# Optimization experiments

Hardware: AMD Instinct MI355X
Metric: run time of the kernel (lower is better)

Reference implementation:

```python
import jax, jax.numpy as jnp
import numpy as np

# dims per module source / chosen globals
B, LB = 4, 28            # new frames, buffered frames; M = B+LB = L = 32
DK, DV = 256, 32         # Dk=256 hardcoded; Dv = 4*len_of_lookup+4 with len_of_lookup=7
HS, WS = 64, 64          # H//8, W//8 with H=W=512
LMAX = 32                # memory cap L
TRAIN_SZ = 1000          # log base train_sz
ALPHA = 0.5              # blend coefficient (original inits 0, which zeroes the branch)
# log(L*h*w + h*w, train_sz) / sqrt(Dk)
SCALE = float(np.log(LMAX * HS * WS + HS * WS) / np.log(TRAIN_SZ) / np.sqrt(DK))


def _xavier(key, fan_in, fan_out):
    lim = np.sqrt(6.0 / (fan_in + fan_out))
    return jax.random.uniform(key, (fan_in, fan_out), jnp.float32, -lim, lim)


def setup_inputs() -> dict:
    key = jax.random.key(0)
    ks = jax.random.split(key, 7)
    return {
        "fc": jax.random.normal(ks[0], (B, DK, HS, WS), jnp.float32),
        "fm": jax.random.normal(ks[1], (B, DV, HS, WS), jnp.float32),
        "key_buffer": jax.random.normal(ks[2], (LB, DK, HS, WS), jnp.float32),
        "value_buffer": jax.random.normal(ks[3], (LB, DV, HS, WS), jnp.float32),
        "Q": _xavier(ks[4], DK, DK),
        "K": _xavier(ks[5], DK, DK),
        "V": _xavier(ks[6], DV, DV),
    }


def reference(fc, fm, key_buffer, value_buffer, Q, K, V):
    # matmul = einsum('ijkl,jm->imkl'): per-pixel channel mixing
    q = jnp.einsum('bdhw,de->behw', fc, Q)                      # [B,Dk,h,w]
    k = jnp.concatenate([jnp.einsum('bdhw,de->behw', fc, K), key_buffer], axis=0)    # [M,Dk,h,w]
    v = jnp.concatenate([jnp.einsum('bdhw,de->behw', fm, V), value_buffer], axis=0)  # [M,Dv,h,w]
    # current_batch (=1) < L, so no slicing of k/v on this step
    scores = SCALE * jnp.einsum('bdhw,mdhw->bmhw', q, k)        # [B,M,h,w]
    attn = jax.nn.softmax(scores, axis=-1)                      # NOTE: softmax over width axis, as in source (dim=-1)
    ctx = jnp.einsum('bmhw,mdhw->bdhw', attn, v)                # [B,Dv,h,w]
    return fm + ALPHA * ctx
```

## Files before the change

### kernel.cpp

```cpp
#include <hip/hip_runtime.h>
#include <hip/hip_bf16.h>
#include <cmath>

#define NB 4
#define NM 32
#define DKc 256
#define DVc 32
#define NP 4096

using bf16x8 = __attribute__((ext_vector_type(8))) short;
using f32x4  = __attribute__((ext_vector_type(4))) float;
using f32x2  = __attribute__((ext_vector_type(2))) float;

__device__ __forceinline__ unsigned short f2bf(float f) {
    union { float f; unsigned u; } x; x.f = f;
    unsigned r = 0x7FFFu + ((x.u >> 16) & 1u);
    return (unsigned short)((x.u + r) >> 16);
}

__global__ __launch_bounds__(256) void k_prep(
    const float* __restrict__ fc, unsigned short* __restrict__ fcT,
    const float* __restrict__ Q, unsigned short* __restrict__ WTq,
    const float* __restrict__ K, unsigned short* __restrict__ WTk,
    const float* __restrict__ fm, const float* __restrict__ V, float* __restrict__ vproj) {
    int x = blockIdx.x;
    int t = threadIdx.x;
    if (x < 1056) {
        __shared__ float tile[64][65];
        const float* s; unsigned short* d; int R, C, r0, c0;
        if (x < 1024) {
            int bb = x >> 8, rest = x & 255;
            R = 256; C = 4096;
            r0 = (rest >> 6) * 64; c0 = (rest & 63) * 64;
            s = fc + (long)bb * 256 * 4096; d = fcT + (long)bb * 256 * 4096;
        } else {
            int i = x - 1024;
            int mat = i >> 4, idx = i & 15;
            R = 256; C = 256;
            r0 = (idx >> 2) * 64; c0 = (idx & 3) * 64;
            s = mat ? K : Q; d = mat ? WTk : WTq;
        }
        #pragma unroll
        for (int j = 0; j < 16; ++j) {
            int i = t + 256 * j;
            int r = i >> 6, c = i & 63;
            tile[r][c] = s[(long)(r0 + r) * C + c0 + c];
        }
        __syncthreads();
        #pragma unroll
        for (int j = 0; j < 8; ++j) {
            int i = t + 256 * j;
            int row = i >> 5;
            int pr = i & 31;
            float f0 = tile[2 * pr][row];
            float f1 = tile[2 * pr + 1][row];
            unsigned pack = (unsigned)f2bf(f0) | ((unsigned)f2bf(f1) << 16);
            reinterpret_cast<unsigned*>(d)[(((long)(c0 + row) * R + r0) >> 1) + pr] = pack;
        }
    } else {
        __shared__ float Vl[32][32];
        __shared__ float fml[32][256];
        int i = x - 1056;
        int b = i >> 4, p0 = (i & 15) * 256;
        #pragma unroll
        for (int j = 0; j < 4; ++j) { int ii = t + 256 * j; Vl[ii >> 5][ii & 31] = V[ii]; }
        for (int j = 0; j < 32; ++j) {
            int ii = t + 256 * j;
            int dd = ii >> 8, c = ii & 255;
            fml[dd][c] = fm[((long)b * DVc + dd) * NP + p0 + c];
        }
        __syncthreads();
        float acc[32];
        #pragma unroll
        for (int e = 0; e < 32; ++e) acc[e] = 0.f;
        for (int dd = 0; dd < 32; ++dd) {
            float fv = fml[dd][t];
            #pragma unroll
            for (int e = 0; e < 32; ++e) acc[e] += fv * Vl[dd][e];
        }
        #pragma unroll
        for (int e = 0; e < 32; ++e) vproj[((long)b * DVc + e) * NP + p0 + t] = acc[e];
    }
}

__global__ __launch_bounds__(256) void k_proj(
    const unsigned short* __restrict__ WTq, const unsigned short* __restrict__ WTk,
    const unsigned short* __restrict__ fcT,
    float* __restrict__ qproj, float* __restrict__ kproj) {
    int t = threadIdx.x;
    int wave = t >> 6, lane = t & 63;
    int y = blockIdx.y;
    int b = y & 3, mat = y >> 2;
    int p0 = blockIdx.x * 64;
    int ln = lane & 15, quad = lane >> 4;
    const unsigned short* WT = mat ? WTk : WTq;
    float* dst = mat ? kproj : qproj;
    int e0w = wave * 64;
    const unsigned short* bbase = fcT + ((long)b * NP + p0 + ln) * DKc + quad * 8;
    f32x4 acc[4][4] = {};
    for (int kk = 0; kk < DKc; kk += 32) {
        bf16x8 a[4], bb[4];
        #pragma unroll
        for (int i = 0; i < 4; ++i)
            a[i] = *reinterpret_cast<const bf16x8*>(WT + (long)(e0w + i * 16 + ln) * DKc + quad * 8 + kk);
        #pragma unroll
        for (int j = 0; j < 4; ++j)
            bb[j] = *reinterpret_cast<const bf16x8*>(bbase + (long)j * 16 * DKc + kk);
        #pragma unroll
        for (int i = 0; i < 4; ++i)
            #pragma unroll
            for (int j = 0; j < 4; ++j)
                acc[i][j] = __builtin_amdgcn_mfma_f32_16x16x32_bf16(a[i], bb[j], acc[i][j], 0, 0, 0);
    }
    #pragma unroll
    for (int i = 0; i < 4; ++i)
        #pragma unroll
        for (int j = 0; j < 4; ++j)
            #pragma unroll
            for (int r = 0; r < 4; ++r) {
                int e = e0w + i * 16 + quad * 4 + r, p = p0 + j * 16 + ln;
                dst[((long)b * DKc + e) * NP + p] = acc[i][j][r];
            }
}

__global__ __launch_bounds__(256, 2) void k_scores(
    const float* __restrict__ qproj, const float* __restrict__ kproj,
    const float* __restrict__ kbuf, float* __restrict__ partial) {
    int t = threadIdx.x;
    int wseg = blockIdx.x, ec = blockIdx.y, mq = blockIdx.z;
    int w0 = wseg * 512 + t * 2;
    int e0 = ec * 32;
    const float* kp[4];
    #pragma unroll
    for (int mi = 0; mi < 4; ++mi) {
        int m = mq * 4 + mi;
        kp[mi] = (m < 4 ? kproj + (long)m * DKc * NP : kbuf + (long)(m - 4) * DKc * NP)
                 + (long)e0 * NP + w0;
    }
    const float* qp[4];
    #pragma unroll
    for (int b = 0; b < 4; ++b)
        qp[b] = qproj + ((long)b * DKc + e0) * NP + w0;

    f32x2 acc[4][4];
    #pragma unroll
    for (int b = 0; b < 4; ++b)
        #pragma unroll
        for (int mi = 0; mi < 4; ++mi) acc[b][mi] = (f32x2){0.f, 0.f};

    for (int e4 = 0; e4 < 32; e4 += 4) {
        f32x2 qv[4][4], kv[4][4];
        #pragma unroll
        for (int u = 0; u < 4; ++u) {
            long off = (long)(e4 + u) * NP;
            #pragma unroll
            for (int b = 0; b < 4; ++b)
                qv[u][b] = *reinterpret_cast<const f32x2*>(qp[b] + off);
            #pragma unroll
            for (int mi = 0; mi < 4; ++mi)
                kv[u][mi] = *reinterpret_cast<const f32x2*>(kp[mi] + off);
        }
        #pragma unroll
        for (int u = 0; u < 4; ++u)
            #pragma unroll
            for (int b = 0; b < 4; ++b)
                #pragma unroll
                for (int mi = 0; mi < 4; ++mi)
                    acc[b][mi] += qv[u][b] * kv[u][mi];
    }
    #pragma unroll
    for (int b = 0; b < 4; ++b)
        #pragma unroll
        for (int mi = 0; mi < 4; ++mi) {
            float* pp = partial + (((long)b * 8 + ec) * NM + mq * 4 + mi) * NP + w0;
            *reinterpret_cast<f32x2*>(pp) = acc[b][mi];
        }
}

__global__ __launch_bounds__(512) void k_out(
    const float* __restrict__ partial, const float* __restrict__ vproj,
    const float* __restrict__ vbuf, const float* __restrict__ fm,
    float* __restrict__ out, float scale) {
    __shared__ float sc[32][68];
    int t = threadIdx.x;
    int b = blockIdx.x >> 6, hrow = blockIdx.x & 63;
    int p0h = hrow * 64;
    int wave = t >> 6, lane = t & 63;
    {
        int w = t & 63, mg = t >> 6;
        float s[4] = {0.f, 0.f, 0.f, 0.f};
        #pragma unroll
        for (int c = 0; c < 8; ++c) {
            const float* pp = partial + (((long)b * 8 + c) * NM + mg * 4) * NP + p0h + w;
            #pragma unroll
            for (int mi = 0; mi < 4; ++mi) s[mi] += pp[(long)mi * NP];
        }
        #pragma unroll
        for (int mi = 0; mi < 4; ++mi) sc[mg * 4 + mi][w] = s[mi] * scale;
    }
    __syncthreads();
    #pragma unroll
    for (int r = 0; r < 4; ++r) {
        int m = wave * 4 + r;
        float x = sc[m][lane];
        float mx = x;
        #pragma unroll
        for (int d = 1; d < 64; d <<= 1) mx = fmaxf(mx, __shfl_xor(mx, d));
        float e = __expf(x - mx);
        float sum = e;
        #pragma unroll
        for (int d = 1; d < 64; d <<= 1) sum += __shfl_xor(sum, d);
        sc[m][lane] = e / sum;
    }
    __syncthreads();
    {
        int dg = t >> 6, w = t & 63;
        float c4[4] = {0.f, 0.f, 0.f, 0.f};
        #pragma unroll
        for (int m = 0; m < NM; ++m) {
            float a = sc[m][w];
            const float* vp = (m < 4 ? vproj + (long)m * DVc * NP : vbuf + (long)(m - 4) * DVc * NP)
                              + (long)(dg * 4) * NP + p0h + w;
            #pragma unroll
            for (int i = 0; i < 4; ++i) c4[i] += a * vp[(long)i * NP];
        }
        #pragma unroll
        for (int i = 0; i < 4; ++i) {
            long gi = ((long)b * DVc + dg * 4 + i) * NP + p0h + w;
            out[gi] = fm[gi] + 0.5f * c4[i];
        }
    }
}

extern "C" void kernel_launch(void* const* d_in, const int* in_sizes, int n_in,
                              void* d_out, int out_size, void* d_ws, size_t ws_size,
                              hipStream_t stream) {
    const float* fc = (const float*)d_in[0];
    const float* fm = (const float*)d_in[1];
    const float* kb = (const float*)d_in[2];
    const float* vb = (const float*)d_in[3];
    const float* Q  = (const float*)d_in[4];
    const float* K  = (const float*)d_in[5];
    const float* V  = (const float*)d_in[6];
    float* out = (float*)d_out;
    char* ws = (char*)d_ws;
    float*          qproj = (float*)(ws);
    float*          kproj = (float*)(ws + 16777216);
    float*          vproj = (float*)(ws + 33554432);
    unsigned short* fcT   = (unsigned short*)(ws + 35651584);
    unsigned short* WTq   = (unsigned short*)(ws + 44040192);
    unsigned short* WTk   = (unsigned short*)(ws + 44171264);
    float*          partial = (float*)(ws + 35651584);
    float scale = (float)(log(135168.0) / log(1000.0) / 16.0);

    hipLaunchKernelGGL(k_prep, dim3(1120), dim3(256), 0, stream,
                       fc, fcT, Q, WTq, K, WTk, fm, V, vproj);
    hipLaunchKernelGGL(k_proj, dim3(64, 8), dim3(256), 0, stream,
                       WTq, WTk, fcT, qproj, kproj);
    hipLaunchKernelGGL(k_scores, dim3(8, 8, 8), dim3(256), 0, stream,
                       qproj, kproj, kb, partial);
    hipLaunchKernelGGL(k_out, dim3(256), dim3(512), 0, stream,
                       partial, vproj, vb, fm, out, scale);
}
```

Measured before the change: 244.5 us.

## Fuse score computation, softmax and value aggregation into a single kernel

Replaces the separate scores kernel, which wrote split-K partial sums to workspace, and the output kernel with one fused kernel. Each 1024-thread block handles one (batch, row) pair. It stages that row's query projection in shared memory and computes the full 256-deep dot products against all 32 memory keys, two keys per wave. It then applies the width softmax and aggregates values. This removes the partial-score round trip through global memory and one launch. The cost is that the key tensors are re-read once per batch index rather than shared across batches, and the grid is only 256 large blocks.

```diff
diff --git a/kernel.cpp b/kernel.cpp
--- a/kernel.cpp
+++ b/kernel.cpp
@@ -123,111 +123,89 @@
             }
 }
 
-__global__ __launch_bounds__(256, 2) void k_scores(
+__global__ __launch_bounds__(1024) void k_fused(
     const float* __restrict__ qproj, const float* __restrict__ kproj,
-    const float* __restrict__ kbuf, float* __restrict__ partial) {
-    int t = threadIdx.x;
-    int wseg = blockIdx.x, ec = blockIdx.y, mq = blockIdx.z;
-    int w0 = wseg * 512 + t * 2;
-    int e0 = ec * 32;
-    const float* kp[4];
-    #pragma unroll
-    for (int mi = 0; mi < 4; ++mi) {
-        int m = mq * 4 + mi;
-        kp[mi] = (m < 4 ? kproj + (long)m * DKc * NP : kbuf + (long)(m - 4) * DKc * NP)
-                 + (long)e0 * NP + w0;
-    }
-    const float* qp[4];
-    #pragma unroll
-    for (int b = 0; b < 4; ++b)
-        qp[b] = qproj + ((long)b * DKc + e0) * NP + w0;
-
-    f32x2 acc[4][4];
-    #pragma unroll
-    for (int b = 0; b < 4; ++b)
-        #pragma unroll
-        for (int mi = 0; mi < 4; ++mi) acc[b][mi] = (f32x2){0.f, 0.f};
-
-    for (int e4 = 0; e4 < 32; e4 += 4) {
-        f32x2 qv[4][4], kv[4][4];
-        #pragma unroll
-        for (int u = 0; u < 4; ++u) {
-            long off = (long)(e4 + u) * NP;
-            #pragma unroll
-            for (int b = 0; b < 4; ++b)
-                qv[u][b] = *reinterpret_cast<const f32x2*>(qp[b] + off);
-            #pragma unroll
-            for (int mi = 0; mi < 4; ++mi)
-                kv[u][mi] = *reinterpret_cast<const f32x2*>(kp[mi] + off);
-        }
-        #pragma unroll
-        for (int u = 0; u < 4; ++u)
-            #pragma unroll
-            for (int b = 0; b < 4; ++b)
-                #pragma unroll
-                for (int mi = 0; mi < 4; ++mi)
-                    acc[b][mi] += qv[u][b] * kv[u][mi];
-    }
-    #pragma unroll
-    for (int b = 0; b < 4; ++b)
-        #pragma unroll
-        for (int mi = 0; mi < 4; ++mi) {
-            float* pp = partial + (((long)b * 8 + ec) * NM + mq * 4 + mi) * NP + w0;
-            *reinterpret_cast<f32x2*>(pp) = acc[b][mi];
-        }
-}
-
-__global__ __launch_bounds__(512) void k_out(
-    const float* __restrict__ partial, const float* __restrict__ vproj,
+    const float* __restrict__ kbuf, const float* __restrict__ vproj,
     const float* __restrict__ vbuf, const float* __restrict__ fm,
     float* __restrict__ out, float scale) {
-    __shared__ float sc[32][68];
+    __shared__ float smem[256 * 64];
     int t = threadIdx.x;
     int b = blockIdx.x >> 6, hrow = blockIdx.x & 63;
-    int p0h = hrow * 64;
+    int p0 = hrow * 64;
     int wave = t >> 6, lane = t & 63;
+
     {
-        int w = t & 63, mg = t >> 6;
-        float s[4] = {0.f, 0.f, 0.f, 0.f};
-        #pragma unroll
-        for (int c = 0; c < 8; ++c) {
-            const float* pp = partial + (((long)b * 8 + c) * NM + mg * 4) * NP + p0h + w;
-            #pragma unroll
-            for (int mi = 0; mi < 4; ++mi) s[mi] += pp[(long)mi * NP];
-        }
-        #pragma unroll
-        for (int mi = 0; mi < 4; ++mi) sc[mg * 4 + mi][w] = s[mi] * scale;
+        const float* qbase = qproj + (long)b * DKc * NP + p0;
+        #pragma unroll
+        for (int j = 0; j < 16; ++j) {
+            int i = t + 1024 * j;
+            int e = i >> 6, w = i & 63;
+            smem[e * 64 + w] = qbase[(long)e * NP + w];
+        }
+    }
+    __syncthreads();
+
+    float attnw[2];
+    {
+        const float* kp[2];
+        #pragma unroll
+        for (int mi = 0; mi < 2; ++mi) {
+            int m = wave * 2 + mi;
+            kp[mi] = (m < 4 ? kproj + (long)m * DKc * NP : kbuf + (long)(m - 4) * DKc * NP)
+                     + p0 + lane;
+        }
+        float s[2] = {0.f, 0.f};
+        for (int e8 = 0; e8 < 256; e8 += 8) {
+            float qv[8], kv[8][2];
+            #pragma unroll
+            for (int u = 0; u < 8; ++u) qv[u] = smem[(e8 + u) * 64 + lane];
+            #pragma unroll
+            for (int u = 0; u < 8; ++u)
+                #pragma unroll
+                for (int mi = 0; mi < 2; ++mi)
+                    kv[u][mi] = kp[mi][(long)u * NP];
+            #pragma unroll
+            for (int u = 0; u < 8; ++u)
+                #pragma unroll
+                for (int mi = 0; mi < 2; ++mi)
+                    s[mi] += qv[u] * kv[u][mi];
+            #pragma unroll
+            for (int mi = 0; mi < 2; ++mi) kp[mi] += 8 * NP;
+        }
+        #pragma unroll
+        for (int mi = 0; mi < 2; ++mi) {
+            float x = s[mi] * scale;
+            float mx = x;
+            #pragma unroll
+            for (int d = 1; d < 64; d <<= 1) mx = fmaxf(mx, __shfl_xor(mx, d));
+            float ev = __expf(x - mx);
+            float sum = ev;
+            #pragma unroll
+            for (int d = 1; d < 64; d <<= 1) sum += __shfl_xor(sum, d);
+            attnw[mi] = ev / sum;
+        }
     }
     __syncthreads();
     #pragma unroll
-    for (int r = 0; r < 4; ++r) {
-        int m = wave * 4 + r;
-        float x = sc[m][lane];
-        float mx = x;
-        #pragma unroll
-        for (int d = 1; d < 64; d <<= 1) mx = fmaxf(mx, __shfl_xor(mx, d));
-        float e = __expf(x - mx);
-        float sum = e;
-        #pragma unroll
-        for (int d = 1; d < 64; d <<= 1) sum += __shfl_xor(sum, d);
-        sc[m][lane] = e / sum;
-    }
+    for (int mi = 0; mi < 2; ++mi)
+        smem[(wave * 2 + mi) * 68 + lane] = attnw[mi];
     __syncthreads();
+
     {
         int dg = t >> 6, w = t & 63;
-        float c4[4] = {0.f, 0.f, 0.f, 0.f};
+        float c2[2] = {0.f, 0.f};
         #pragma unroll
         for (int m = 0; m < NM; ++m) {
-            float a = sc[m][w];
+            float a = smem[m * 68 + w];
             const float* vp = (m < 4 ? vproj + (long)m * DVc * NP : vbuf + (long)(m - 4) * DVc * NP)
-                              + (long)(dg * 4) * NP + p0h + w;
-            #pragma unroll
-            for (int i = 0; i < 4; ++i) c4[i] += a * vp[(long)i * NP];
-        }
-        #pragma unroll
-        for (int i = 0; i < 4; ++i) {
-            long gi = ((long)b * DVc + dg * 4 + i) * NP + p0h + w;
-            out[gi] = fm[gi] + 0.5f * c4[i];
+                              + (long)(dg * 2) * NP + p0 + w;
+            #pragma unroll
+            for (int i = 0; i < 2; ++i) c2[i] += a * vp[(long)i * NP];
+        }
+        #pragma unroll
+        for (int i = 0; i < 2; ++i) {
+            long gi = ((long)b * DVc + dg * 2 + i) * NP + p0 + w;
+            out[gi] = fm[gi] + 0.5f * c2[i];
         }
     }
 }
@@ -250,15 +228,12 @@
     unsigned short* fcT   = (unsigned short*)(ws + 35651584);
     unsigned short* WTq   = (unsigned short*)(ws + 44040192);
     unsigned short* WTk   = (unsigned short*)(ws + 44171264);
-    float*          partial = (float*)(ws + 35651584);
     float scale = (float)(log(135168.0) / log(1000.0) / 16.0);
 
     hipLaunchKernelGGL(k_prep, dim3(1120), dim3(256), 0, stream,
                        fc, fcT, Q, WTq, K, WTk, fm, V, vproj);
     hipLaunchKernelGGL(k_proj, dim3(64, 8), dim3(256), 0, stream,
                        WTq, WTk, fcT, qproj, kproj);
-    hipLaunchKernelGGL(k_scores, dim3(8, 8, 8), dim3(256), 0, stream,
-                       qproj, kproj, kb, partial);
-    hipLaunchKernelGGL(k_out, dim3(256), dim3(512), 0, stream,
-                       partial, vproj, vb, fm, out, scale);
-}
+    hipLaunchKernelGGL(k_fused, dim3(256), dim3(1024), 0, stream,
+                       qproj, kproj, kb, vproj, vb, fm, out, scale);
+}
```

Measured after the change: 252.6 us. 3.3% more time.

## Restructure scores kernel with async global-to-LDS double buffering and in-block reduction

Applied to the files above, without the earlier changes.

Rewrites the scores kernel so each block covers a 64-pixel segment, four memory frames and the full key dimension. Key slabs are streamed into double-buffered LDS through global_load_lds, and the split-K partials are reduced in shared memory inside the block. This removes the 8-way partial-sum buffer and its reduction in the output kernel, which cuts global traffic. In exchange the grid becomes 512 blocks with heavy LDS use and a barrier every iteration, and the query loads are scalar reads of 4 bytes.

```diff
diff --git a/kernel.cpp b/kernel.cpp
--- a/kernel.cpp
+++ b/kernel.cpp
@@ -16,6 +16,14 @@
     union { float f; unsigned u; } x; x.f = f;
     unsigned r = 0x7FFFu + ((x.u >> 16) & 1u);
     return (unsigned short)((x.u + r) >> 16);
+}
+
+typedef const unsigned int __attribute__((address_space(1)))* gas1_t;
+typedef unsigned int __attribute__((address_space(3)))* las3_t;
+__device__ __forceinline__ void glds16(const float* g, float* l) {
+    __builtin_amdgcn_global_load_lds((gas1_t)(const unsigned int*)g,
+                                     (las3_t)(unsigned int*)l,
+                                     16, 0, 0);
 }
 
 __global__ __launch_bounds__(256) void k_prep(
@@ -123,62 +131,75 @@
             }
 }
 
-__global__ __launch_bounds__(256, 2) void k_scores(
+__global__ __launch_bounds__(256) void k_scores(
     const float* __restrict__ qproj, const float* __restrict__ kproj,
-    const float* __restrict__ kbuf, float* __restrict__ partial) {
-    int t = threadIdx.x;
-    int wseg = blockIdx.x, ec = blockIdx.y, mq = blockIdx.z;
-    int w0 = wseg * 512 + t * 2;
-    int e0 = ec * 32;
-    const float* kp[4];
-    #pragma unroll
-    for (int mi = 0; mi < 4; ++mi) {
-        int m = mq * 4 + mi;
-        kp[mi] = (m < 4 ? kproj + (long)m * DKc * NP : kbuf + (long)(m - 4) * DKc * NP)
-                 + (long)e0 * NP + w0;
-    }
-    const float* qp[4];
+    const float* __restrict__ kbuf, float* __restrict__ scores) {
+    __shared__ float kst[2][2048];
+    __shared__ float red[4096];
+    int t = threadIdx.x;
+    int w = t & 63, es = t >> 6;
+    int wseg = blockIdx.x, mq = blockIdx.y;
+    int w0 = wseg * 64;
+    const size_t KMS = (size_t)DKc * NP;
+
+    const float* kslab = (mq == 0 ? kproj + (size_t)es * KMS
+                                  : kbuf + (size_t)(mq * 4 + es - 4) * KMS);
+    const float* g0 = kslab + (size_t)(w >> 4) * NP + w0 + (w & 15) * 4;
+
+    const float* qb = qproj;
+    float acc[4][4];
     #pragma unroll
     for (int b = 0; b < 4; ++b)
-        qp[b] = qproj + ((long)b * DKc + e0) * NP + w0;
-
-    f32x2 acc[4][4];
+        #pragma unroll
+        for (int m = 0; m < 4; ++m) acc[b][m] = 0.f;
+
+    glds16(g0,            &kst[0][es * 512]);
+    glds16(g0 + 4 * NP,   &kst[0][es * 512 + 256]);
+    __syncthreads();
+
+    for (int it = 0; it < 32; ++it) {
+        int cur = it & 1;
+        if (it < 31) {
+            const float* gn = g0 + (size_t)(it + 1) * 8 * NP;
+            glds16(gn,          &kst[cur ^ 1][es * 512]);
+            glds16(gn + 4 * NP, &kst[cur ^ 1][es * 512 + 256]);
+        }
+        int e0g = it * 8 + es * 2;
+        float qv[4][2];
+        #pragma unroll
+        for (int b = 0; b < 4; ++b) {
+            const float* qp = qb + ((size_t)(b * DKc) + e0g) * NP + w0 + w;
+            qv[b][0] = qp[0];
+            qv[b][1] = qp[NP];
+        }
+        #pragma unroll
+        for (int m = 0; m < 4; ++m) {
+            float k0 = kst[cur][(m * 8 + es * 2) * 64 + w];
+            float k1 = kst[cur][(m * 8 + es * 2 + 1) * 64 + w];
+            #pragma unroll
+            for (int b = 0; b < 4; ++b)
+                acc[b][m] = fmaf(qv[b][0], k0, fmaf(qv[b][1], k1, acc[b][m]));
+        }
+        __syncthreads();
+    }
+
     #pragma unroll
     for (int b = 0; b < 4; ++b)
         #pragma unroll
-        for (int mi = 0; mi < 4; ++mi) acc[b][mi] = (f32x2){0.f, 0.f};
-
-    for (int e4 = 0; e4 < 32; e4 += 4) {
-        f32x2 qv[4][4], kv[4][4];
-        #pragma unroll
-        for (int u = 0; u < 4; ++u) {
-            long off = (long)(e4 + u) * NP;
-            #pragma unroll
-            for (int b = 0; b < 4; ++b)
-                qv[u][b] = *reinterpret_cast<const f32x2*>(qp[b] + off);
-            #pragma unroll
-            for (int mi = 0; mi < 4; ++mi)
-                kv[u][mi] = *reinterpret_cast<const f32x2*>(kp[mi] + off);
-        }
-        #pragma unroll
-        for (int u = 0; u < 4; ++u)
-            #pragma unroll
-            for (int b = 0; b < 4; ++b)
-                #pragma unroll
-                for (int mi = 0; mi < 4; ++mi)
-                    acc[b][mi] += qv[u][b] * kv[u][mi];
-    }
-    #pragma unroll
-    for (int b = 0; b < 4; ++b)
-        #pragma unroll
-        for (int mi = 0; mi < 4; ++mi) {
-            float* pp = partial + (((long)b * 8 + ec) * NM + mq * 4 + mi) * NP + w0;
-            *reinterpret_cast<f32x2*>(pp) = acc[b][mi];
-        }
+        for (int m = 0; m < 4; ++m)
+            red[es * 1024 + (b * 4 + m) * 64 + w] = acc[b][m];
+    __syncthreads();
+    #pragma unroll
+    for (int j = 0; j < 4; ++j) {
+        int idx = t + 256 * j;
+        float v = red[idx] + red[1024 + idx] + red[2048 + idx] + red[3072 + idx];
+        int b = idx >> 8, m = (idx >> 6) & 3, w2 = idx & 63;
+        scores[((size_t)b * NM + mq * 4 + m) * NP + w0 + w2] = v;
+    }
 }
 
 __global__ __launch_bounds__(512) void k_out(
-    const float* __restrict__ partial, const float* __restrict__ vproj,
+    const float* __restrict__ scores, const float* __restrict__ vproj,
     const float* __restrict__ vbuf, const float* __restrict__ fm,
     float* __restrict__ out, float scale) {
     __shared__ float sc[32][68];
@@ -186,17 +207,11 @@
     int b = blockIdx.x >> 6, hrow = blockIdx.x & 63;
     int p0h = hrow * 64;
     int wave = t >> 6, lane = t & 63;
-    {
-        int w = t & 63, mg = t >> 6;
-        float s[4] = {0.f, 0.f, 0.f, 0.f};
-        #pragma unroll
-        for (int c = 0; c < 8; ++c) {
-            const float* pp = partial + (((long)b * 8 + c) * NM + mg * 4) * NP + p0h + w;
-            #pragma unroll
-            for (int mi = 0; mi < 4; ++mi) s[mi] += pp[(long)mi * NP];
-        }
-        #pragma unroll
-        for (int mi = 0; mi < 4; ++mi) sc[mg * 4 + mi][w] = s[mi] * scale;
+    #pragma unroll
+    for (int j = 0; j < 4; ++j) {
+        int idx = t + 512 * j;
+        int m = idx >> 6, w = idx & 63;
+        sc[m][w] = scores[((size_t)b * NM + m) * NP + p0h + w] * scale;
     }
     __syncthreads();
     #pragma unroll
@@ -244,21 +259,21 @@
     const float* V  = (const float*)d_in[6];
     float* out = (float*)d_out;
     char* ws = (char*)d_ws;
-    float*          qproj = (float*)(ws);
-    float*          kproj = (float*)(ws + 16777216);
-    float*          vproj = (float*)(ws + 33554432);
-    unsigned short* fcT   = (unsigned short*)(ws + 35651584);
-    unsigned short* WTq   = (unsigned short*)(ws + 44040192);
-    unsigned short* WTk   = (unsigned short*)(ws + 44171264);
-    float*          partial = (float*)(ws + 35651584);
+    float*          qproj  = (float*)(ws);
+    float*          kproj  = (float*)(ws + 16777216);
+    float*          vproj  = (float*)(ws + 33554432);
+    unsigned short* fcT    = (unsigned short*)(ws + 35651584);
+    unsigned short* WTq    = (unsigned short*)(ws + 44040192);
+    unsigned short* WTk    = (unsigned short*)(ws + 44171264);
+    float*          scores = (float*)(ws + 35651584);
     float scale = (float)(log(135168.0) / log(1000.0) / 16.0);
 
     hipLaunchKernelGGL(k_prep, dim3(1120), dim3(256), 0, stream,
                        fc, fcT, Q, WTq, K, WTk, fm, V, vproj);
     hipLaunchKernelGGL(k_proj, dim3(64, 8), dim3(256), 0, stream,
                        WTq, WTk, fcT, qproj, kproj);
-    hipLaunchKernelGGL(k_scores, dim3(8, 8, 8), dim3(256), 0, stream,
-                       qproj, kproj, kb, partial);
+    hipLaunchKernelGGL(k_scores, dim3(64, 8), dim3(256), 0, stream,
+                       qproj, kproj, kb, scores);
     hipLaunchKernelGGL(k_out, dim3(256), dim3(512), 0, stream,
-                       partial, vproj, vb, fm, out, scale);
-}
+                       scores, vproj, vb, fm, out, scale);
+}
```

New measurement: 238.2 us. 1.03x faster.
